# Optimization experiments

Hardware: AMD Instinct MI355X
Metric: run time of the kernel (lower is better)

## Reference

```python
import jax, jax.numpy as jnp
import numpy as np

K = 8192      # num_embeddings
D = 512       # embedding_dim
DECAY = 0.99
EPS = 1e-5


def setup_inputs() -> dict:
    key = jax.random.key(0)
    k1, k2, k3 = jax.random.split(key, 3)
    inputs = jax.random.normal(k1, (8, 2048, D), dtype=jnp.float32)
    weight = jax.random.normal(k2, (K, D), dtype=jnp.float32) * 0.01
    ema_cluster_size = jnp.ones((K,), dtype=jnp.float32)
    ema_w = jax.random.normal(k3, (K, D), dtype=jnp.float32) * 0.01
    return {"inputs": inputs, "weight": weight,
            "ema_cluster_size": ema_cluster_size, "ema_w": ema_w}


def _l2norm(x):
    return x / jnp.sqrt(jnp.sum(x * x, axis=-1, keepdims=True) + 1e-12)


def reference(inputs, weight, ema_cluster_size, ema_w):
    # Flatten tokens: [N, D]
    flat = inputs.reshape(-1, D)
    cb = _l2norm(weight)            # [K, D]
    xn = _l2norm(flat)              # [N, D]
    # distances = 2 - 2 * sim; argmin(dist) == argmax(sim)
    sim = jnp.einsum('nd,kd->nk', xn, cb)          # [N, K]
    idx = jnp.argmax(sim, axis=1)                  # [N]
    # quantized = one_hot(idx) @ weight  ==  gather
    quantized = weight[idx].reshape(inputs.shape)
    # EMA codebook update (training path)
    counts = jax.ops.segment_sum(jnp.ones_like(idx, dtype=inputs.dtype), idx,
                                 num_segments=K)   # one_hot.sum(0)
    new_cs = ema_cluster_size * DECAY + (1.0 - DECAY) * counts
    n = jnp.sum(new_cs)
    new_cs = (new_cs + EPS) / (n + K * EPS) * n
    dw = jax.ops.segment_sum(flat, idx, num_segments=K)  # one_hot.T @ flat
    new_ema_w = ema_w * DECAY + (1.0 - DECAY) * dw
    new_weight = new_ema_w / new_cs[:, None]
    # Commitment loss and straight-through estimator
    e_latent_loss = jnp.mean((jax.lax.stop_gradient(quantized) - inputs) ** 2)
    quantized_st = inputs + jax.lax.stop_gradient(quantized - inputs)
    return (quantized_st, e_latent_loss, idx[:, None],
            new_cs, new_ema_w, new_weight)
```

## Files before the change

kernel.cpp:

```cpp
#include <hip/hip_runtime.h>
#include <cstdint>
#include <cstddef>

#define NTOK 16384
#define DIM  512
#define KCB  8192
#define MARGIN 6.0e-3f
#define LISTCAP 512

typedef short s16x8 __attribute__((ext_vector_type(8)));
typedef float f32x4 __attribute__((ext_vector_type(4)));

static const size_t WS_XN   = 0;
static const size_t WS_WN   = 16777216;
static const size_t WS_KV   = 25165824;
static const size_t WS_LP   = 37748736;
static const size_t WS_PRE  = 37814272;
static const size_t WS_N    = 37847040;
static const size_t WS_CNT  = 37847296;
static const size_t WS_LIST = 37880064;

__device__ __forceinline__ void gl_lds16(const void* g, void* l) {
  __builtin_amdgcn_global_load_lds(
      (__attribute__((address_space(1))) void*)(uintptr_t)g,
      (__attribute__((address_space(3))) void*)(uint32_t)(uintptr_t)l,
      16, 0, 0);
}

__device__ __forceinline__ unsigned short f2bf(float f) {
  unsigned int u = __float_as_uint(f);
  u = (u + 0x7fffu + ((u >> 16) & 1u)) >> 16;
  return (unsigned short)u;
}

__global__ __launch_bounds__(256) void k_normalize(const float* __restrict__ x,
                                                   const float* __restrict__ w,
                                                   unsigned short* __restrict__ xn,
                                                   unsigned short* __restrict__ wn) {
  const int row = blockIdx.x;
  const int tid = threadIdx.x, lane = tid & 63, wave = tid >> 6;
  const float* src;
  unsigned short* dst;
  if (row < NTOK) { src = x + (size_t)row * DIM;          dst = xn + (size_t)row * DIM; }
  else            { src = w + (size_t)(row - NTOK) * DIM; dst = wn + (size_t)(row - NTOK) * DIM; }
  const int e = tid * 2;
  float2 v = *(const float2*)(src + e);
  float ss = v.x * v.x + v.y * v.y;
  #pragma unroll
  for (int off = 32; off > 0; off >>= 1) ss += __shfl_xor(ss, off);
  __shared__ float red[4];
  if (lane == 0) red[wave] = ss;
  __syncthreads();
  const float s = red[0] + red[1] + red[2] + red[3];
  const float inv = rsqrtf(s + 1e-12f);
  unsigned int lo = f2bf(v.x * inv), hi = f2bf(v.y * inv);
  *(unsigned int*)(dst + e) = lo | (hi << 16);
}

__global__ __launch_bounds__(256, 2) void k_gemm_top2(const unsigned short* __restrict__ xn,
                                                      const unsigned short* __restrict__ wn,
                                                      uint2* __restrict__ kv) {
  __shared__ __align__(16) unsigned short smA[128 * 64];
  __shared__ __align__(16) unsigned short smB[256 * 64];
  const int tid = threadIdx.x, wave = tid >> 6, lane = tid & 63;
  const int quad = lane >> 4, col = lane & 15;
  const int wave_m = (wave & 1) * 64, wave_n = (wave >> 1) * 128;
  const int n0 = blockIdx.x * 256, m0 = blockIdx.y * 128;

  const unsigned short* pA[4];
  const unsigned short* pB[8];
  unsigned short* dA[4];
  unsigned short* dB[8];
  #pragma unroll
  for (int i = 0; i < 4; ++i) {
    int s = wave * 256 + i * 64 + lane;
    int row = s >> 3, cg = (s & 7) ^ (row & 7);
    pA[i] = xn + (size_t)(m0 + row) * DIM + cg * 8;
    dA[i] = &smA[(size_t)(wave * 256 + i * 64) * 8];
  }
  #pragma unroll
  for (int i = 0; i < 8; ++i) {
    int s = wave * 512 + i * 64 + lane;
    int row = s >> 3, cg = (s & 7) ^ (row & 7);
    pB[i] = wn + (size_t)(n0 + row) * DIM + cg * 8;
    dB[i] = &smB[(size_t)(wave * 512 + i * 64) * 8];
  }

  int offA[4][2], offB[8][2];
  #pragma unroll
  for (int kbi = 0; kbi < 2; ++kbi) {
    int kb = kbi * 4 + quad;
    #pragma unroll
    for (int mi = 0; mi < 4; ++mi) {
      int row = wave_m + mi * 16 + col;
      offA[mi][kbi] = (row * 8 + (kb ^ (row & 7))) * 16;
    }
    #pragma unroll
    for (int ni = 0; ni < 8; ++ni) {
      int row = wave_n + ni * 16 + col;
      offB[ni][kbi] = (row * 8 + (kb ^ (row & 7))) * 16;
    }
  }

  f32x4 acc[4][8] = {};
  const char* sA = (const char*)smA;
  const char* sB = (const char*)smB;

  #pragma unroll 1
  for (int kt = 0; kt < 8; ++kt) {
    __syncthreads();
    #pragma unroll
    for (int i = 0; i < 4; ++i) { gl_lds16(pA[i], dA[i]); pA[i] += 64; }
    #pragma unroll
    for (int i = 0; i < 8; ++i) { gl_lds16(pB[i], dB[i]); pB[i] += 64; }
    __syncthreads();
    #pragma unroll
    for (int kbi = 0; kbi < 2; ++kbi) {
      s16x8 af[4], bfr[8];
      #pragma unroll
      for (int mi = 0; mi < 4; ++mi) af[mi]  = *(const s16x8*)(sA + offA[mi][kbi]);
      #pragma unroll
      for (int ni = 0; ni < 8; ++ni) bfr[ni] = *(const s16x8*)(sB + offB[ni][kbi]);
      #pragma unroll
      for (int mi = 0; mi < 4; ++mi)
        #pragma unroll
        for (int ni = 0; ni < 8; ++ni)
          acc[mi][ni] = __builtin_amdgcn_mfma_f32_16x16x32_bf16(af[mi], bfr[ni], acc[mi][ni], 0, 0, 0);
    }
  }

  const int tile = blockIdx.x * 2 + (wave >> 1);
  unsigned int rk1 = 0, rk2 = 0;
  #pragma unroll
  for (int mi = 0; mi < 4; ++mi) {
    #pragma unroll
    for (int r = 0; r < 4; ++r) {
      const int p = mi * 4 + r;
      unsigned int k1 = 0, k2 = 0;
      #pragma unroll
      for (int ni = 0; ni < 8; ++ni) {
        float vb = acc[mi][ni][r] + 2.0f;
        unsigned int key = (__float_as_uint(vb) & ~0x7Fu) | (unsigned int)(ni * 16 + col);
        unsigned int mn = min(k1, key);
        k1 = max(k1, key);
        k2 = max(k2, mn);
      }
      #pragma unroll
      for (int off = 1; off < 16; off <<= 1) {
        unsigned int o1 = (unsigned int)__shfl_xor((int)k1, off);
        unsigned int o2 = (unsigned int)__shfl_xor((int)k2, off);
        unsigned int mn = min(k1, o1);
        k1 = max(k1, o1);
        k2 = max(max(k2, o2), mn);
      }
      if (col == p) { rk1 = k1; rk2 = k2; }
    }
  }
  const int row = wave_m + (col >> 2) * 16 + quad * 4 + (col & 3);
  kv[(size_t)(m0 + row) * 64 + tile] = make_uint2(rk1, rk2);
}

__global__ __launch_bounds__(256) void k_select(const float* __restrict__ x,
                                                const float* __restrict__ wgt,
                                                const uint2* __restrict__ kv,
                                                float* __restrict__ out0,
                                                float* __restrict__ out_idx,
                                                float* __restrict__ lp,
                                                int* __restrict__ cnt,
                                                int* __restrict__ list) {
  const int wave = threadIdx.x >> 6, lane = threadIdx.x & 63;
  const int t = blockIdx.x * 4 + wave;

  const uint2 kp = kv[(size_t)t * 64 + lane];
  const float v1 = __uint_as_float(kp.x);
  const float v2 = __uint_as_float(kp.y);
  const int   i1 = lane * 128 + (int)(kp.x & 0x7Fu);

  float gm = v1;
  #pragma unroll
  for (int off = 32; off > 0; off >>= 1) gm = fmaxf(gm, __shfl_xor(gm, off));
  const float thresh = gm - MARGIN;

  unsigned long long m1 = __ballot(v1 >= thresh);
  unsigned long long m2 = __ballot(v2 >= thresh);

  const float* xrow = x + (size_t)t * DIM;
  const float* xr = xrow + lane * 8;
  float4 x0 = *(const float4*)xr;
  float4 x1 = *(const float4*)(xr + 4);
  double xv[8] = {x0.x, x0.y, x0.z, x0.w, x1.x, x1.y, x1.z, x1.w};

  double bestv = -1e300; int besti = 1 << 30;

  auto evalc = [&](int c) {
    const float* wr = wgt + (size_t)c * DIM + lane * 8;
    float4 w0 = *(const float4*)wr;
    float4 w1 = *(const float4*)(wr + 4);
    double s  = (double)w0.x * xv[0] + (double)w0.y * xv[1] + (double)w0.z * xv[2] + (double)w0.w * xv[3]
              + (double)w1.x * xv[4] + (double)w1.y * xv[5] + (double)w1.z * xv[6] + (double)w1.w * xv[7];
    double nw = (double)w0.x * w0.x + (double)w0.y * w0.y + (double)w0.z * w0.z + (double)w0.w * w0.w
              + (double)w1.x * w1.x + (double)w1.y * w1.y + (double)w1.z * w1.z + (double)w1.w * w1.w;
    #pragma unroll
    for (int off = 1; off < 64; off <<= 1) { s += __shfl_xor(s, off); nw += __shfl_xor(nw, off); }
    double sim = s / sqrt(nw + 1e-12);
    if (sim > bestv || (sim == bestv && c < besti)) { bestv = sim; besti = c; }
  };

  while (m1) {
    int b = __builtin_ctzll(m1); m1 &= m1 - 1;
    evalc(__shfl(i1, b));
  }
  while (m2) {
    int b = __builtin_ctzll(m2); m2 &= m2 - 1;
    #pragma unroll 1
    for (int chunk = 0; chunk < 2; ++chunk) {
      const int c = b * 128 + chunk * 64 + lane;
      const float* wr = wgt + (size_t)c * DIM;
      double s = 0.0, nw = 0.0;
      #pragma unroll 4
      for (int d = 0; d < DIM; d += 4) {
        float4 wv = *(const float4*)(wr + d);
        float4 xw = *(const float4*)(xrow + d);
        s  += (double)wv.x * xw.x + (double)wv.y * xw.y + (double)wv.z * xw.z + (double)wv.w * xw.w;
        nw += (double)wv.x * wv.x + (double)wv.y * wv.y + (double)wv.z * wv.z + (double)wv.w * wv.w;
      }
      double sim = s / sqrt(nw + 1e-12);
      if (sim > bestv || (sim == bestv && c < besti)) { bestv = sim; besti = c; }
    }
  }
  #pragma unroll
  for (int off = 1; off < 64; off <<= 1) {
    double ov = __shfl_xor(bestv, off);
    int    oi = __shfl_xor(besti, off);
    if (ov > bestv || (ov == bestv && oi < besti)) { bestv = ov; besti = oi; }
  }
  if ((unsigned)besti >= KCB) besti = 0;

  const float* wr = wgt + (size_t)besti * DIM + lane * 8;
  float4 w0 = *(const float4*)wr;
  float4 w1 = *(const float4*)(wr + 4);
  float* o0 = out0 + (size_t)t * DIM + lane * 8;
  *(float4*)o0 = w0;
  *(float4*)(o0 + 4) = w1;
  double d2 = 0.0;
  double qv[8] = {w0.x, w0.y, w0.z, w0.w, w1.x, w1.y, w1.z, w1.w};
  #pragma unroll
  for (int j = 0; j < 8; ++j) { double d = qv[j] - xv[j]; d2 += d * d; }
  #pragma unroll
  for (int off = 1; off < 64; off <<= 1) d2 += __shfl_xor(d2, off);

  if (lane == 0) {
    lp[t] = (float)d2;
    out_idx[t] = (float)besti;
    int slot = atomicAdd(&cnt[besti], 1);
    if (slot < LISTCAP) list[besti * LISTCAP + slot] = t;
  }
}

__global__ __launch_bounds__(256) void k_scalars(const float* __restrict__ cs,
                                                 const int* __restrict__ cnt,
                                                 float* __restrict__ pre,
                                                 const float* __restrict__ lp,
                                                 double* __restrict__ nacc,
                                                 float* __restrict__ out1) {
  __shared__ double red[256];
  const int tid = threadIdx.x;
  double s = 0.0;
  for (int i = tid * 4; i < KCB; i += 1024) {
    float4 c4 = *(const float4*)(cs + i);
    int4   n4 = *(const int4*)(cnt + i);
    float p0 = c4.x * 0.99f + 0.01f * (float)n4.x;
    float p1 = c4.y * 0.99f + 0.01f * (float)n4.y;
    float p2 = c4.z * 0.99f + 0.01f * (float)n4.z;
    float p3 = c4.w * 0.99f + 0.01f * (float)n4.w;
    *(float4*)(pre + i) = make_float4(p0, p1, p2, p3);
    s += (double)p0 + (double)p1 + (double)p2 + (double)p3;
  }
  red[tid] = s; __syncthreads();
  for (int st = 128; st > 0; st >>= 1) { if (tid < st) red[tid] += red[tid + st]; __syncthreads(); }
  if (tid == 0) *nacc = red[0];
  __syncthreads();
  double l = 0.0;
  for (int i = tid * 4; i < NTOK; i += 1024) {
    float4 l4 = *(const float4*)(lp + i);
    l += (double)l4.x + (double)l4.y + (double)l4.z + (double)l4.w;
  }
  red[tid] = l; __syncthreads();
  for (int st = 128; st > 0; st >>= 1) { if (tid < st) red[tid] += red[tid + st]; __syncthreads(); }
  if (tid == 0) out1[0] = (float)(red[0] / (double)((size_t)NTOK * DIM));
}

__global__ __launch_bounds__(256) void k_dw(const float* __restrict__ x,
                                            const float* __restrict__ ema_w,
                                            const int* __restrict__ cnt,
                                            const int* __restrict__ list,
                                            const float* __restrict__ pre,
                                            const double* __restrict__ nacc,
                                            float* __restrict__ out3,
                                            float* __restrict__ out4,
                                            float* __restrict__ out5) {
  const int c = blockIdx.x, tid = threadIdx.x;
  int m = cnt[c]; if (m > LISTCAP) m = LISTCAP;
  const double n = *nacc;
  const float csf = (float)(((double)pre[c] + 1e-5) / (n + (double)KCB * 1e-5) * n);
  const int d0 = tid * 2;
  double s0 = 0.0, s1 = 0.0;
  for (int j = 0; j < m; ++j) {
    int t = list[c * LISTCAP + j] & (NTOK - 1);
    float2 v = *(const float2*)(x + (size_t)t * DIM + d0);
    s0 += (double)v.x; s1 += (double)v.y;
  }
  const size_t e = (size_t)c * DIM + d0;
  float n0 = ema_w[e]     * 0.99f + 0.01f * (float)s0;
  float n1 = ema_w[e + 1] * 0.99f + 0.01f * (float)s1;
  out4[e] = n0;       out4[e + 1] = n1;
  out5[e] = n0 / csf; out5[e + 1] = n1 / csf;
  if (tid == 0) out3[c] = csf;
}

extern "C" void kernel_launch(void* const* d_in, const int* in_sizes, int n_in,
                              void* d_out, int out_size, void* d_ws, size_t ws_size,
                              hipStream_t stream) {
  const float* x    = (const float*)d_in[0];
  const float* wgt  = (const float*)d_in[1];
  const float* cs   = (const float*)d_in[2];
  const float* emaw = (const float*)d_in[3];

  char* ws = (char*)d_ws;
  unsigned short* xn  = (unsigned short*)(ws + WS_XN);
  unsigned short* wn  = (unsigned short*)(ws + WS_WN);
  uint2* kv    = (uint2*)(ws + WS_KV);
  float* lp    = (float*)(ws + WS_LP);
  float* pre   = (float*)(ws + WS_PRE);
  double* nacc = (double*)(ws + WS_N);
  int*   cnt   = (int*)(ws + WS_CNT);
  int*   list  = (int*)(ws + WS_LIST);

  float* out0 = (float*)d_out;
  float* out1 = out0 + 8388608;
  float* out2 = out1 + 1;
  float* out3 = out2 + NTOK;
  float* out4 = out3 + KCB;
  float* out5 = out4 + (size_t)KCB * DIM;

  hipMemsetAsync(cnt, 0, KCB * sizeof(int), stream);

  k_normalize<<<NTOK + KCB, 256, 0, stream>>>(x, wgt, xn, wn);
  k_gemm_top2<<<dim3(32, 128), 256, 0, stream>>>(xn, wn, kv);
  k_select<<<NTOK / 4, 256, 0, stream>>>(x, wgt, kv, out0, out2, lp, cnt, list);
  k_scalars<<<1, 256, 0, stream>>>(cs, cnt, pre, lp, nacc, out1);
  k_dw<<<KCB, 256, 0, stream>>>(x, emaw, cnt, list, pre, nacc, out3, out4, out5);
}
```

Before: 366.9 us.

## Double-buffer GEMM tiles with 256x256 blocks and ping-pong phased MFMA scheduling

Rewrites the similarity GEMM main loop to use 512-thread blocks computing 256x256 tiles. Global-to-LDS loads are double-buffered so the next K-slice of A and B is prefetched while MFMAs run on the current one. Work is split into barrier-separated phases with explicit waitcnt and setprio to interleave loads with matrix math. This aims to hide memory latency and increase data reuse per block, at the cost of 128KB of LDS per block (lower occupancy) and fragile hand-written synchronisation.

```diff
diff --git a/kernel.cpp b/kernel.cpp
--- a/kernel.cpp
+++ b/kernel.cpp
@@ -57,79 +57,105 @@
   *(unsigned int*)(dst + e) = lo | (hi << 16);
 }
 
-__global__ __launch_bounds__(256, 2) void k_gemm_top2(const unsigned short* __restrict__ xn,
+#define SBAR()  asm volatile("s_barrier" ::: "memory")
+#define LGKM0() do { asm volatile("s_waitcnt lgkmcnt(0)" ::: "memory"); \
+                     __builtin_amdgcn_sched_barrier(0); } while (0)
+#define VMW(N)  asm volatile("s_waitcnt vmcnt(" #N ")" ::: "memory")
+
+__global__ __launch_bounds__(512, 2) void k_gemm_top2(const unsigned short* __restrict__ xn,
                                                       const unsigned short* __restrict__ wn,
                                                       uint2* __restrict__ kv) {
-  __shared__ __align__(16) unsigned short smA[128 * 64];
-  __shared__ __align__(16) unsigned short smB[256 * 64];
+  __shared__ __align__(16) char lds[131072];
+  char* const ldsA = lds;
+  char* const ldsB = lds + 65536;
   const int tid = threadIdx.x, wave = tid >> 6, lane = tid & 63;
   const int quad = lane >> 4, col = lane & 15;
-  const int wave_m = (wave & 1) * 64, wave_n = (wave >> 1) * 128;
-  const int n0 = blockIdx.x * 256, m0 = blockIdx.y * 128;
-
-  const unsigned short* pA[4];
-  const unsigned short* pB[8];
-  unsigned short* dA[4];
-  unsigned short* dB[8];
-  #pragma unroll
-  for (int i = 0; i < 4; ++i) {
-    int s = wave * 256 + i * 64 + lane;
-    int row = s >> 3, cg = (s & 7) ^ (row & 7);
-    pA[i] = xn + (size_t)(m0 + row) * DIM + cg * 8;
-    dA[i] = &smA[(size_t)(wave * 256 + i * 64) * 8];
-  }
-  #pragma unroll
-  for (int i = 0; i < 8; ++i) {
-    int s = wave * 512 + i * 64 + lane;
-    int row = s >> 3, cg = (s & 7) ^ (row & 7);
-    pB[i] = wn + (size_t)(n0 + row) * DIM + cg * 8;
-    dB[i] = &smB[(size_t)(wave * 512 + i * 64) * 8];
-  }
-
-  int offA[4][2], offB[8][2];
-  #pragma unroll
-  for (int kbi = 0; kbi < 2; ++kbi) {
-    int kb = kbi * 4 + quad;
+  const int wave_m = (wave & 3) * 64;
+  const int wave_n = (wave >> 2) * 128;
+  const int n0 = blockIdx.x * 256, m0 = blockIdx.y * 256;
+
+  const int seg0 = wave * 128 + lane;
+  const int r0 = seg0 >> 3, cg0 = (seg0 & 7) ^ (r0 & 7);
+  const int seg1 = seg0 + 64;
+  const int r1 = seg1 >> 3, cg1 = (seg1 & 7) ^ (r1 & 7);
+  const unsigned short* const pA0 = xn + (size_t)(m0 + r0) * DIM + cg0 * 8;
+  const unsigned short* const pA1 = xn + (size_t)(m0 + r1) * DIM + cg1 * 8;
+  const unsigned short* const pB0 = wn + (size_t)(n0 + r0) * DIM + cg0 * 8;
+  const unsigned short* const pB1 = wn + (size_t)(n0 + r1) * DIM + cg1 * 8;
+  const int dj0 = wave * 2048;
+
+#define STAGE_A(HALF, KT) do { \
+    char* da_ = ldsA + (((KT) & 1) << 15) + ((HALF) << 14) + dj0; \
+    gl_lds16(pA0 + (HALF) * 65536 + (KT) * 64, da_); \
+    gl_lds16(pA1 + (HALF) * 65536 + (KT) * 64, da_ + 1024); \
+  } while (0)
+#define STAGE_B(HALF, KT) do { \
+    char* db_ = ldsB + (((KT) & 1) << 15) + ((HALF) << 14) + dj0; \
+    gl_lds16(pB0 + (HALF) * 65536 + (KT) * 64, db_); \
+    gl_lds16(pB1 + (HALF) * 65536 + (KT) * 64, db_ + 1024); \
+  } while (0)
+
+  int offA[4], offB[8];
+  #pragma unroll
+  for (int mi = 0; mi < 4; ++mi) {
+    int row = wave_m + mi * 16 + col;
+    offA[mi] = (row >> 7) * 16384 + (row & 127) * 128 + ((quad ^ (row & 7)) * 16);
+  }
+  #pragma unroll
+  for (int ni = 0; ni < 8; ++ni) {
+    int row = wave_n + ni * 16 + col;
+    offB[ni] = (row >> 7) * 16384 + (row & 127) * 128 + ((quad ^ (row & 7)) * 16);
+  }
+
+  f32x4 acc[4][8] = {};
+  s16x8 af[4][2];
+
+#define PHASE(KBI, NB, STAGE_STMT, TAIL_STMT) do {                                   \
+    s16x8 bfr0 = *(const s16x8*)(ldsB + bufoff + (offB[(NB) + 0] ^ ((KBI) * 64)));   \
+    s16x8 bfr1 = *(const s16x8*)(ldsB + bufoff + (offB[(NB) + 1] ^ ((KBI) * 64)));   \
+    s16x8 bfr2 = *(const s16x8*)(ldsB + bufoff + (offB[(NB) + 2] ^ ((KBI) * 64)));   \
+    s16x8 bfr3 = *(const s16x8*)(ldsB + bufoff + (offB[(NB) + 3] ^ ((KBI) * 64)));   \
+    STAGE_STMT;                                                                      \
+    SBAR();                                                                          \
+    LGKM0();                                                                         \
+    __builtin_amdgcn_s_setprio(1);                                                   \
+    _Pragma("unroll")                                                                \
+    for (int mi = 0; mi < 4; ++mi) {                                                 \
+      acc[mi][(NB) + 0] = __builtin_amdgcn_mfma_f32_16x16x32_bf16(af[mi][KBI], bfr0, acc[mi][(NB) + 0], 0, 0, 0); \
+      acc[mi][(NB) + 1] = __builtin_amdgcn_mfma_f32_16x16x32_bf16(af[mi][KBI], bfr1, acc[mi][(NB) + 1], 0, 0, 0); \
+      acc[mi][(NB) + 2] = __builtin_amdgcn_mfma_f32_16x16x32_bf16(af[mi][KBI], bfr2, acc[mi][(NB) + 2], 0, 0, 0); \
+      acc[mi][(NB) + 3] = __builtin_amdgcn_mfma_f32_16x16x32_bf16(af[mi][KBI], bfr3, acc[mi][(NB) + 3], 0, 0, 0); \
+    }                                                                                \
+    __builtin_amdgcn_s_setprio(0);                                                   \
+    TAIL_STMT;                                                                       \
+    SBAR();                                                                          \
+  } while (0)
+
+  STAGE_A(0, 0); STAGE_A(1, 0); STAGE_B(0, 0); STAGE_B(1, 0);
+  STAGE_A(0, 1); STAGE_A(1, 1);
+  VMW(4);
+  SBAR();
+
+  #pragma unroll 1
+  for (int t = 0; t < 8; ++t) {
+    const int bufoff = (t & 1) << 15;
     #pragma unroll
     for (int mi = 0; mi < 4; ++mi) {
-      int row = wave_m + mi * 16 + col;
-      offA[mi][kbi] = (row * 8 + (kb ^ (row & 7))) * 16;
+      af[mi][0] = *(const s16x8*)(ldsA + bufoff + offA[mi]);
+      af[mi][1] = *(const s16x8*)(ldsA + bufoff + (offA[mi] ^ 64));
     }
-    #pragma unroll
-    for (int ni = 0; ni < 8; ++ni) {
-      int row = wave_n + ni * 16 + col;
-      offB[ni][kbi] = (row * 8 + (kb ^ (row & 7))) * 16;
-    }
-  }
-
-  f32x4 acc[4][8] = {};
-  const char* sA = (const char*)smA;
-  const char* sB = (const char*)smB;
-
-  #pragma unroll 1
-  for (int kt = 0; kt < 8; ++kt) {
-    __syncthreads();
-    #pragma unroll
-    for (int i = 0; i < 4; ++i) { gl_lds16(pA[i], dA[i]); pA[i] += 64; }
-    #pragma unroll
-    for (int i = 0; i < 8; ++i) { gl_lds16(pB[i], dB[i]); pB[i] += 64; }
-    __syncthreads();
-    #pragma unroll
-    for (int kbi = 0; kbi < 2; ++kbi) {
-      s16x8 af[4], bfr[8];
-      #pragma unroll
-      for (int mi = 0; mi < 4; ++mi) af[mi]  = *(const s16x8*)(sA + offA[mi][kbi]);
-      #pragma unroll
-      for (int ni = 0; ni < 8; ++ni) bfr[ni] = *(const s16x8*)(sB + offB[ni][kbi]);
-      #pragma unroll
-      for (int mi = 0; mi < 4; ++mi)
-        #pragma unroll
-        for (int ni = 0; ni < 8; ++ni)
-          acc[mi][ni] = __builtin_amdgcn_mfma_f32_16x16x32_bf16(af[mi], bfr[ni], acc[mi][ni], 0, 0, 0);
-    }
-  }
-
-  const int tile = blockIdx.x * 2 + (wave >> 1);
+    PHASE(0, 0, if (t < 7) STAGE_B(0, t + 1), );
+    PHASE(0, 4, if (t < 7) STAGE_B(1, t + 1), );
+    PHASE(1, 0, if (t < 6) STAGE_A(0, t + 2), );
+    PHASE(1, 4, if (t < 6) STAGE_A(1, t + 2),
+          if (t < 6) { VMW(4); } else if (t == 6) { VMW(0); });
+  }
+
+#undef PHASE
+#undef STAGE_A
+#undef STAGE_B
+
+  const int tile = blockIdx.x * 2 + (wave >> 2);
   unsigned int rk1 = 0, rk2 = 0;
   #pragma unroll
   for (int mi = 0; mi < 4; ++mi) {
@@ -346,7 +372,7 @@
   hipMemsetAsync(cnt, 0, KCB * sizeof(int), stream);
 
   k_normalize<<<NTOK + KCB, 256, 0, stream>>>(x, wgt, xn, wn);
-  k_gemm_top2<<<dim3(32, 128), 256, 0, stream>>>(xn, wn, kv);
+  k_gemm_top2<<<dim3(32, 64), 512, 0, stream>>>(xn, wn, kv);
   k_select<<<NTOK / 4, 256, 0, stream>>>(x, wgt, kv, out0, out2, lp, cnt, list);
   k_scalars<<<1, 256, 0, stream>>>(cs, cnt, pre, lp, nacc, out1);
   k_dw<<<KCB, 256, 0, stream>>>(x, emaw, cnt, list, pre, nacc, out3, out4, out5);
```

New measurement: 374.6 us. 2.1% more time.

## Skip exact rescoring for unambiguous tokens and parallelize scalar reductions

Applied to the files above, without the earlier changes.

In the selection kernel, tokens with exactly one candidate above the margin threshold take the approximate winner directly and skip the fp64 rescoring loop and cross-lane argmax reduction. The single-block scalar kernel becomes 32 blocks using wave shuffles and double atomics. It uses the identity that the counts sum to the token count, so the cluster-size sum is 0.99*sum(cs)+0.01*NTOK, and per-cluster pre-values are recomputed in k_dw instead of stored. This trades a slightly different summation order and atomic nondeterminism for less serial work and one fewer buffer round trip.

```diff
diff --git a/kernel.cpp b/kernel.cpp
--- a/kernel.cpp
+++ b/kernel.cpp
@@ -15,7 +15,6 @@
 static const size_t WS_WN   = 16777216;
 static const size_t WS_KV   = 25165824;
 static const size_t WS_LP   = 37748736;
-static const size_t WS_PRE  = 37814272;
 static const size_t WS_N    = 37847040;
 static const size_t WS_CNT  = 37847296;
 static const size_t WS_LIST = 37880064;
@@ -190,49 +189,56 @@
   float4 x1 = *(const float4*)(xr + 4);
   double xv[8] = {x0.x, x0.y, x0.z, x0.w, x1.x, x1.y, x1.z, x1.w};
 
-  double bestv = -1e300; int besti = 1 << 30;
-
-  auto evalc = [&](int c) {
-    const float* wr = wgt + (size_t)c * DIM + lane * 8;
-    float4 w0 = *(const float4*)wr;
-    float4 w1 = *(const float4*)(wr + 4);
-    double s  = (double)w0.x * xv[0] + (double)w0.y * xv[1] + (double)w0.z * xv[2] + (double)w0.w * xv[3]
-              + (double)w1.x * xv[4] + (double)w1.y * xv[5] + (double)w1.z * xv[6] + (double)w1.w * xv[7];
-    double nw = (double)w0.x * w0.x + (double)w0.y * w0.y + (double)w0.z * w0.z + (double)w0.w * w0.w
-              + (double)w1.x * w1.x + (double)w1.y * w1.y + (double)w1.z * w1.z + (double)w1.w * w1.w;
-    #pragma unroll
-    for (int off = 1; off < 64; off <<= 1) { s += __shfl_xor(s, off); nw += __shfl_xor(nw, off); }
-    double sim = s / sqrt(nw + 1e-12);
-    if (sim > bestv || (sim == bestv && c < besti)) { bestv = sim; besti = c; }
-  };
-
-  while (m1) {
-    int b = __builtin_ctzll(m1); m1 &= m1 - 1;
-    evalc(__shfl(i1, b));
-  }
-  while (m2) {
-    int b = __builtin_ctzll(m2); m2 &= m2 - 1;
-    #pragma unroll 1
-    for (int chunk = 0; chunk < 2; ++chunk) {
-      const int c = b * 128 + chunk * 64 + lane;
-      const float* wr = wgt + (size_t)c * DIM;
-      double s = 0.0, nw = 0.0;
-      #pragma unroll 4
-      for (int d = 0; d < DIM; d += 4) {
-        float4 wv = *(const float4*)(wr + d);
-        float4 xw = *(const float4*)(xrow + d);
-        s  += (double)wv.x * xw.x + (double)wv.y * xw.y + (double)wv.z * xw.z + (double)wv.w * xw.w;
-        nw += (double)wv.x * wv.x + (double)wv.y * wv.y + (double)wv.z * wv.z + (double)wv.w * wv.w;
-      }
+  int besti;
+  if (__popcll(m1) == 1 && m2 == 0ull) {
+    besti = __shfl(i1, __builtin_ctzll(m1));
+  } else {
+    double bestv = -1e300; besti = 1 << 30;
+
+    auto evalc = [&](int c) {
+      const float* wr = wgt + (size_t)c * DIM + lane * 8;
+      float4 w0 = *(const float4*)wr;
+      float4 w1 = *(const float4*)(wr + 4);
+      double s  = (double)w0.x * xv[0] + (double)w0.y * xv[1] + (double)w0.z * xv[2] + (double)w0.w * xv[3]
+                + (double)w1.x * xv[4] + (double)w1.y * xv[5] + (double)w1.z * xv[6] + (double)w1.w * xv[7];
+      double nw = (double)w0.x * w0.x + (double)w0.y * w0.y + (double)w0.z * w0.z + (double)w0.w * w0.w
+                + (double)w1.x * w1.x + (double)w1.y * w1.y + (double)w1.z * w1.z + (double)w1.w * w1.w;
+      #pragma unroll
+      for (int off = 1; off < 64; off <<= 1) { s += __shfl_xor(s, off); nw += __shfl_xor(nw, off); }
       double sim = s / sqrt(nw + 1e-12);
       if (sim > bestv || (sim == bestv && c < besti)) { bestv = sim; besti = c; }
-    }
-  }
-  #pragma unroll
-  for (int off = 1; off < 64; off <<= 1) {
-    double ov = __shfl_xor(bestv, off);
-    int    oi = __shfl_xor(besti, off);
-    if (ov > bestv || (ov == bestv && oi < besti)) { bestv = ov; besti = oi; }
+    };
+
+    unsigned long long w1m = m1;
+    while (w1m) {
+      int b = __builtin_ctzll(w1m); w1m &= w1m - 1;
+      evalc(__shfl(i1, b));
+    }
+    unsigned long long w2m = m2;
+    while (w2m) {
+      int b = __builtin_ctzll(w2m); w2m &= w2m - 1;
+      #pragma unroll 1
+      for (int chunk = 0; chunk < 2; ++chunk) {
+        const int c = b * 128 + chunk * 64 + lane;
+        const float* wr = wgt + (size_t)c * DIM;
+        double s = 0.0, nw = 0.0;
+        #pragma unroll 4
+        for (int d = 0; d < DIM; d += 4) {
+          float4 wv = *(const float4*)(wr + d);
+          float4 xw = *(const float4*)(xrow + d);
+          s  += (double)wv.x * xw.x + (double)wv.y * xw.y + (double)wv.z * xw.z + (double)wv.w * xw.w;
+          nw += (double)wv.x * wv.x + (double)wv.y * wv.y + (double)wv.z * wv.z + (double)wv.w * wv.w;
+        }
+        double sim = s / sqrt(nw + 1e-12);
+        if (sim > bestv || (sim == bestv && c < besti)) { bestv = sim; besti = c; }
+      }
+    }
+    #pragma unroll
+    for (int off = 1; off < 64; off <<= 1) {
+      double ov = __shfl_xor(bestv, off);
+      int    oi = __shfl_xor(besti, off);
+      if (ov > bestv || (ov == bestv && oi < besti)) { bestv = ov; besti = oi; }
+    }
   }
   if ((unsigned)besti >= KCB) besti = 0;
 
@@ -258,51 +264,43 @@
 }
 
 __global__ __launch_bounds__(256) void k_scalars(const float* __restrict__ cs,
-                                                 const int* __restrict__ cnt,
-                                                 float* __restrict__ pre,
                                                  const float* __restrict__ lp,
                                                  double* __restrict__ nacc,
-                                                 float* __restrict__ out1) {
-  __shared__ double red[256];
-  const int tid = threadIdx.x;
-  double s = 0.0;
-  for (int i = tid * 4; i < KCB; i += 1024) {
-    float4 c4 = *(const float4*)(cs + i);
-    int4   n4 = *(const int4*)(cnt + i);
-    float p0 = c4.x * 0.99f + 0.01f * (float)n4.x;
-    float p1 = c4.y * 0.99f + 0.01f * (float)n4.y;
-    float p2 = c4.z * 0.99f + 0.01f * (float)n4.z;
-    float p3 = c4.w * 0.99f + 0.01f * (float)n4.w;
-    *(float4*)(pre + i) = make_float4(p0, p1, p2, p3);
-    s += (double)p0 + (double)p1 + (double)p2 + (double)p3;
-  }
-  red[tid] = s; __syncthreads();
-  for (int st = 128; st > 0; st >>= 1) { if (tid < st) red[tid] += red[tid + st]; __syncthreads(); }
-  if (tid == 0) *nacc = red[0];
+                                                 double* __restrict__ lacc) {
+  const int tid = threadIdx.x, b = blockIdx.x;
+  const int wave = tid >> 6, lane = tid & 63;
+  double s = (double)cs[b * 256 + tid];
+  float2 l2 = *(const float2*)(lp + b * 512 + tid * 2);
+  double l = (double)l2.x + (double)l2.y;
+  #pragma unroll
+  for (int off = 32; off > 0; off >>= 1) { s += __shfl_xor(s, off); l += __shfl_xor(l, off); }
+  __shared__ double rs[4], rl[4];
+  if (lane == 0) { rs[wave] = s; rl[wave] = l; }
   __syncthreads();
-  double l = 0.0;
-  for (int i = tid * 4; i < NTOK; i += 1024) {
-    float4 l4 = *(const float4*)(lp + i);
-    l += (double)l4.x + (double)l4.y + (double)l4.z + (double)l4.w;
-  }
-  red[tid] = l; __syncthreads();
-  for (int st = 128; st > 0; st >>= 1) { if (tid < st) red[tid] += red[tid + st]; __syncthreads(); }
-  if (tid == 0) out1[0] = (float)(red[0] / (double)((size_t)NTOK * DIM));
+  if (tid == 0) {
+    atomicAdd(nacc, 0.99 * (rs[0] + rs[1] + rs[2] + rs[3]));
+    atomicAdd(lacc, rl[0] + rl[1] + rl[2] + rl[3]);
+  }
 }
 
 __global__ __launch_bounds__(256) void k_dw(const float* __restrict__ x,
                                             const float* __restrict__ ema_w,
+                                            const float* __restrict__ cs,
                                             const int* __restrict__ cnt,
                                             const int* __restrict__ list,
-                                            const float* __restrict__ pre,
                                             const double* __restrict__ nacc,
+                                            const double* __restrict__ lacc,
+                                            float* __restrict__ out1,
                                             float* __restrict__ out3,
                                             float* __restrict__ out4,
                                             float* __restrict__ out5) {
   const int c = blockIdx.x, tid = threadIdx.x;
-  int m = cnt[c]; if (m > LISTCAP) m = LISTCAP;
-  const double n = *nacc;
-  const float csf = (float)(((double)pre[c] + 1e-5) / (n + (double)KCB * 1e-5) * n);
+  const int mtrue = cnt[c];
+  const int m = mtrue > LISTCAP ? LISTCAP : mtrue;
+  const double n = *nacc + 0.01 * (double)NTOK;
+  const float prec = cs[c] * 0.99f + 0.01f * (float)mtrue;
+  const float csf = (float)(((double)prec + 1e-5) / (n + (double)KCB * 1e-5) * n);
+  if (c == 0 && tid == 0) out1[0] = (float)(*lacc / (double)((size_t)NTOK * DIM));
   const int d0 = tid * 2;
   double s0 = 0.0, s1 = 0.0;
   for (int j = 0; j < m; ++j) {
@@ -331,8 +329,8 @@
   unsigned short* wn  = (unsigned short*)(ws + WS_WN);
   uint2* kv    = (uint2*)(ws + WS_KV);
   float* lp    = (float*)(ws + WS_LP);
-  float* pre   = (float*)(ws + WS_PRE);
   double* nacc = (double*)(ws + WS_N);
+  double* lacc = nacc + 1;
   int*   cnt   = (int*)(ws + WS_CNT);
   int*   list  = (int*)(ws + WS_LIST);
 
@@ -344,10 +342,11 @@
   float* out5 = out4 + (size_t)KCB * DIM;
 
   hipMemsetAsync(cnt, 0, KCB * sizeof(int), stream);
+  hipMemsetAsync(ws + WS_N, 0, 2 * sizeof(double), stream);
 
   k_normalize<<<NTOK + KCB, 256, 0, stream>>>(x, wgt, xn, wn);
   k_gemm_top2<<<dim3(32, 128), 256, 0, stream>>>(xn, wn, kv);
   k_select<<<NTOK / 4, 256, 0, stream>>>(x, wgt, kv, out0, out2, lp, cnt, list);
-  k_scalars<<<1, 256, 0, stream>>>(cs, cnt, pre, lp, nacc, out1);
-  k_dw<<<KCB, 256, 0, stream>>>(x, emaw, cnt, list, pre, nacc, out3, out4, out5);
-}
+  k_scalars<<<32, 256, 0, stream>>>(cs, lp, nacc, lacc);
+  k_dw<<<KCB, 256, 0, stream>>>(x, emaw, cs, cnt, list, nacc, lacc, out1, out3, out4, out5);
+}
```

Result: faster. 347.5 us (-5.3%).
